# Performance work log

Measured on AMD Instinct MI355X. Metric: run time of the kernel, lower is better.

## Reference

```python
import jax, jax.numpy as jnp
import numpy as np

NEG = jnp.float32(-1e30)  # log-space 'zero' (avoids -inf NaNs)


def _ctc_loss(predictions, targets, pred_lengths, target_lengths, blank=0):
    # predictions: (B, T, C) log-probs; targets: (B, L) int labels (no blanks)
    B, T, C = predictions.shape
    L = targets.shape[1]
    S = 2 * L + 1  # extended label sequence: blank-interleaved

    ext = jnp.full((B, S), blank, dtype=targets.dtype).at[:, 1::2].set(targets)  # (B, S)
    # emission log-prob of each lattice state at each time step: (B, T, S)
    emit = jnp.take_along_axis(
        predictions, jnp.broadcast_to(ext[:, None, :], (B, T, S)), axis=2)

    # skip transition (s-2 -> s) allowed iff ext[s] != blank and ext[s] != ext[s-2]
    ext_m2 = jnp.pad(ext, ((0, 0), (2, 0)), constant_values=-1)[:, :S]
    skip = (ext != blank) & (ext != ext_m2)  # (B, S)

    alpha0 = jnp.full((B, S), NEG, dtype=predictions.dtype)
    alpha0 = alpha0.at[:, 0].set(emit[:, 0, 0]).at[:, 1].set(emit[:, 0, 1])

    emit_t = jnp.swapaxes(emit, 0, 1)  # (T, B, S)
    pad1 = jnp.full((B, 1), NEG, dtype=predictions.dtype)
    pad2 = jnp.full((B, 2), NEG, dtype=predictions.dtype)

    def step(alpha, xs):
        e_t, t = xs
        a1 = alpha
        a2 = jnp.concatenate([pad1, alpha[:, :-1]], axis=1)
        a3 = jnp.where(skip, jnp.concatenate([pad2, alpha[:, :-2]], axis=1), NEG)
        new = jax.nn.logsumexp(jnp.stack([a1, a2, a3], axis=0), axis=0) + e_t
        # freeze lattice beyond each example's input length
        new = jnp.where((t < pred_lengths)[:, None], new, alpha)
        return new, None

    alpha_T, _ = jax.lax.scan(step, alpha0, (emit_t[1:], jnp.arange(1, T)))

    tl = target_lengths.astype(jnp.int32)
    l1 = jnp.take_along_axis(alpha_T, (2 * tl - 1)[:, None], axis=1)[:, 0]
    l2 = jnp.take_along_axis(alpha_T, (2 * tl)[:, None], axis=1)[:, 0]
    per_ex = -jnp.logaddexp(l1, l2)
    # zero_infinity=True
    per_ex = jnp.where(per_ex > jnp.float32(1e29), 0.0, per_ex)
    # reduction='mean': divide by target length, then batch mean
    return jnp.mean(per_ex / jnp.maximum(tl, 1).astype(per_ex.dtype))


def setup_inputs() -> dict:
    key = jax.random.key(0)
    k1, k2, k3 = jax.random.split(key, 3)
    B, T, C, L = 128, 1024, 128, 128
    predictions = jax.random.normal(k1, (B, T, C), dtype=jnp.float32)
    targets = jax.random.randint(k2, (B, L), 1, C, dtype=jnp.int32)  # no blank (=0)
    pred_lengths = jnp.full((B,), T, dtype=jnp.int32)
    target_lengths = jax.random.randint(k3, (B,), L // 2, L + 1, dtype=jnp.int32)
    return {"predictions": predictions, "targets": targets,
            "pred_lengths": pred_lengths, "target_lengths": target_lengths}


def reference(predictions, targets, pred_lengths, target_lengths):
    return _ctc_loss(predictions, targets, pred_lengths, target_lengths, blank=0)
```

## Files before the change

kernel.cpp:

```cpp
#include <hip/hip_runtime.h>


static constexpr float LOG2E_F = 1.4426950408889634f;
static constexpr float LN2_F   = 0.6931471805599453f;
#define NEGF (-1.0e30f)

#if __has_builtin(__builtin_amdgcn_exp2f)
#define FEXP2(x) __builtin_amdgcn_exp2f(x)
#else
#define FEXP2(x) exp2f(x)
#endif
#if __has_builtin(__builtin_amdgcn_logf)
#define FLOG2(x) __builtin_amdgcn_logf(x)
#else
#define FLOG2(x) log2f(x)
#endif

typedef __attribute__((address_space(3))) uint32_t lds_u32_t;
typedef const __attribute__((address_space(1))) uint32_t glb_u32_t;

__device__ __forceinline__ float dpp_shr1(float src, float fill) {
  return __int_as_float(__builtin_amdgcn_update_dpp(
      __float_as_int(fill), __float_as_int(src), 0x138, 0xF, 0xF, false));
}

template <int T, int C, int L>
__global__ __launch_bounds__(64) void ctc_alpha_dpp(
    const float* __restrict__ pred,
    const int*   __restrict__ targets,
    const int*   __restrict__ pred_len,
    const int*   __restrict__ tgt_len,
    float*       __restrict__ per_ex)
{
  constexpr int ROWS    = 64;
  constexpr int CHUNK_F = ROWS * C;
  constexpr int NCH     = T / ROWS;
  constexpr int S       = 2 * L + 1;

  __shared__ float emis[3 * CHUNK_F];
  __shared__ float afin[S];

  const int b = blockIdx.x;
  const int l = threadIdx.x;

  const float* __restrict__ prow = pred + (size_t)b * T * C;
  const int plen = pred_len[b];
  int tl = tgt_len[b]; if (tl < 1) tl = 1; if (tl > L) tl = L;

  const int cc1 = targets[b * L + 2 * l];
  const int cc3 = targets[b * L + 2 * l + 1];
  const bool skip1 = (l == 0) ? false : (cc1 != targets[b * L + 2 * l - 1]);
  const bool skip3 = (cc3 != cc1);

  auto stage = [&](int c) {
    const float* src0 = prow + (size_t)c * CHUNK_F + (l << 2);
    float* dst0 = &emis[(c % 3) * CHUNK_F];
#pragma unroll
    for (int i = 0; i < 32; ++i) {
      __builtin_amdgcn_global_load_lds((glb_u32_t*)(src0 + (i << 8)),
                                       (lds_u32_t*)(dst0 + (i << 8)),
                                       16, 0, 0);
    }
  };

  stage(0); stage(1);
  asm volatile("s_waitcnt vmcnt(32)" ::: "memory");

  float a0 = emis[0] * LOG2E_F;
  float x1 = (l == 0) ? emis[cc1] * LOG2E_F : NEGF;
  float x2 = NEGF, x3 = NEGF, x4 = NEGF;

  const int tmax = plen < T ? plen : T;

  auto step = [&](float rEb, float rE1, float rE3) {
    const float Eb = rEb * LOG2E_F;
    const float E1 = rE1 * LOG2E_F;
    const float E3 = rE3 * LOG2E_F;
    const float P4 = dpp_shr1(x4, a0);
    const float P3 = dpp_shr1(x3, NEGF);
    const float s1 = skip1 ? P3 : NEGF;
    const float m1 = fmaxf(fmaxf(x1, P4), s1);
    const float n1 = m1 + FLOG2(FEXP2(x1 - m1) + FEXP2(P4 - m1) + FEXP2(s1 - m1)) + E1;
    const float m2 = fmaxf(x2, x1);
    const float n2 = m2 + FLOG2(1.0f + FEXP2(-fabsf(x2 - x1))) + Eb;
    const float s3 = skip3 ? x1 : NEGF;
    const float m3 = fmaxf(fmaxf(x3, x2), s3);
    const float n3 = m3 + FLOG2(FEXP2(x3 - m3) + FEXP2(x2 - m3) + FEXP2(s3 - m3)) + E3;
    const float m4 = fmaxf(x4, x3);
    const float n4 = m4 + FLOG2(1.0f + FEXP2(-fabsf(x4 - x3))) + Eb;
    a0 += Eb;
    x1 = n1; x2 = n2; x3 = n3; x4 = n4;
  };

  auto loadg = [&](float (&gb)[8], float (&g1)[8], float (&g3)[8], int r0) {
#pragma unroll
    for (int j = 0; j < 8; ++j) {
      int rr = r0 + j; if (rr > T - 1) rr = T - 1;
      const int rb = ((rr >> 6) % 3) * CHUNK_F + (rr & 63) * C;
      gb[j] = emis[rb];
      g1[j] = emis[rb + cc1];
      g3[j] = emis[rb + cc3];
    }
  };

#pragma unroll
  for (int t = 1; t < 8; ++t) {
    if (t < tmax) {
      const int rb = t * C;
      step(emis[rb], emis[rb + cc1], emis[rb + cc3]);
    }
  }

  float Ab[8], A1[8], A3[8], Bb[8], B1[8], B3[8];
  loadg(Ab, A1, A3, 8);

  for (int t0 = 8; t0 + 16 <= T; t0 += 16) {
    if ((t0 & 63) == 8) {
      const int c = t0 >> 6;
      if (c + 2 < NCH) {
        stage(c + 2);
        asm volatile("s_waitcnt vmcnt(32)" ::: "memory");
      } else {
        asm volatile("s_waitcnt vmcnt(0)" ::: "memory");
      }
    }
    loadg(Bb, B1, B3, t0 + 8);
    if (t0 + 16 <= tmax) {
#pragma unroll
      for (int j = 0; j < 8; ++j) step(Ab[j], A1[j], A3[j]);
      loadg(Ab, A1, A3, t0 + 16);
#pragma unroll
      for (int j = 0; j < 8; ++j) step(Bb[j], B1[j], B3[j]);
    } else {
#pragma unroll
      for (int j = 0; j < 8; ++j)
        if (t0 + j < tmax) step(Ab[j], A1[j], A3[j]);
      loadg(Ab, A1, A3, t0 + 16);
#pragma unroll
      for (int j = 0; j < 8; ++j)
        if (t0 + 8 + j < tmax) step(Bb[j], B1[j], B3[j]);
    }
  }

  afin[4 * l + 1] = x1;
  afin[4 * l + 2] = x2;
  afin[4 * l + 3] = x3;
  afin[4 * l + 4] = x4;
  if (l == 0) afin[0] = a0;
  __syncthreads();
  if (l == 0) {
    const float l1 = afin[2 * tl - 1];
    const float l2 = afin[2 * tl];
    const float mm = fmaxf(l1, l2);
    const float ls = mm + FLOG2(FEXP2(l1 - mm) + FEXP2(l2 - mm));
    float per = -(ls * LN2_F);
    if (!(per < 1e29f)) per = 0.0f;
    per_ex[b] = per / (float)tl;
  }
}

__global__ void ctc_reduce_kernel(const float* __restrict__ per_ex,
                                  float* __restrict__ out, int B)
{
  const int l = threadIdx.x;
  float v = 0.0f;
  for (int i = l; i < B; i += 64) v += per_ex[i];
#pragma unroll
  for (int off = 32; off > 0; off >>= 1) v += __shfl_down(v, off);
  if (l == 0) out[0] = v / (float)B;
}

extern "C" void kernel_launch(void* const* d_in, const int* in_sizes, int n_in,
                              void* d_out, int out_size, void* d_ws, size_t ws_size,
                              hipStream_t stream)
{
  const float* pred    = (const float*)d_in[0];
  const int*   targets = (const int*)d_in[1];
  const int*   plen    = (const int*)d_in[2];
  const int*   tlen    = (const int*)d_in[3];
  float*       out     = (float*)d_out;
  float*       ws      = (float*)d_ws;

  constexpr int B = 128, T = 1024, C = 128, L = 128;

  hipLaunchKernelGGL((ctc_alpha_dpp<T, C, L>), dim3(B), dim3(64), 0, stream,
                     pred, targets, plen, tlen, ws);
  hipLaunchKernelGGL(ctc_reduce_kernel, dim3(1), dim3(64), 0, stream,
                     ws, out, B);
}
```

Before: 218.2 us.

## Run CTC alpha recursion in linear space with per-lane power-of-two exponents

Replaces the log-space logsumexp recursion with linear-probability products and sums. Each lane keeps an integer exponent, and the state is renormalized every 8 steps. Neighbour values arriving over DPP are rescaled by the exponent difference between lanes. This is meant to take the exp2/log2 transcendentals off the serial dependency chain, leaving only the exp of the emissions, which is not on the chain. The cost is extra bookkeeping for the exponents and a risk of underflow or precision loss if scales between lanes differ widely within a renorm window.

```diff
diff --git a/kernel.cpp b/kernel.cpp
--- a/kernel.cpp
+++ b/kernel.cpp
@@ -3,7 +3,6 @@
 
 static constexpr float LOG2E_F = 1.4426950408889634f;
 static constexpr float LN2_F   = 0.6931471805599453f;
-#define NEGF (-1.0e30f)
 
 #if __has_builtin(__builtin_amdgcn_exp2f)
 #define FEXP2(x) __builtin_amdgcn_exp2f(x)
@@ -23,9 +22,12 @@
   return __int_as_float(__builtin_amdgcn_update_dpp(
       __float_as_int(fill), __float_as_int(src), 0x138, 0xF, 0xF, false));
 }
+__device__ __forceinline__ int dpp_shr1_i(int src, int fill) {
+  return __builtin_amdgcn_update_dpp(fill, src, 0x138, 0xF, 0xF, false);
+}
 
 template <int T, int C, int L>
-__global__ __launch_bounds__(64) void ctc_alpha_dpp(
+__global__ __launch_bounds__(64) void ctc_alpha_lin2(
     const float* __restrict__ pred,
     const int*   __restrict__ targets,
     const int*   __restrict__ pred_len,
@@ -49,8 +51,9 @@
 
   const int cc1 = targets[b * L + 2 * l];
   const int cc3 = targets[b * L + 2 * l + 1];
-  const bool skip1 = (l == 0) ? false : (cc1 != targets[b * L + 2 * l - 1]);
-  const bool skip3 = (cc3 != cc1);
+  const float k1 = (l == 0) ? 0.0f
+                  : ((cc1 != targets[b * L + 2 * l - 1]) ? 1.0f : 0.0f);
+  const float k3 = (cc3 != cc1) ? 1.0f : 0.0f;
 
   auto stage = [&](int c) {
     const float* src0 = prow + (size_t)c * CHUNK_F + (l << 2);
@@ -66,30 +69,38 @@
   stage(0); stage(1);
   asm volatile("s_waitcnt vmcnt(32)" ::: "memory");
 
-  float a0 = emis[0] * LOG2E_F;
-  float x1 = (l == 0) ? emis[cc1] * LOG2E_F : NEGF;
-  float x2 = NEGF, x3 = NEGF, x4 = NEGF;
+  float a0 = FEXP2(emis[0] * LOG2E_F);
+  float x1 = (l == 0) ? FEXP2(emis[cc1] * LOG2E_F) : 0.0f;
+  float x2 = 0.0f, x3 = 0.0f, x4 = 0.0f;
+  int   E  = 0;
 
   const int tmax = plen < T ? plen : T;
 
-  auto step = [&](float rEb, float rE1, float rE3) {
-    const float Eb = rEb * LOG2E_F;
-    const float E1 = rE1 * LOG2E_F;
-    const float E3 = rE3 * LOG2E_F;
-    const float P4 = dpp_shr1(x4, a0);
-    const float P3 = dpp_shr1(x3, NEGF);
-    const float s1 = skip1 ? P3 : NEGF;
-    const float m1 = fmaxf(fmaxf(x1, P4), s1);
-    const float n1 = m1 + FLOG2(FEXP2(x1 - m1) + FEXP2(P4 - m1) + FEXP2(s1 - m1)) + E1;
-    const float m2 = fmaxf(x2, x1);
-    const float n2 = m2 + FLOG2(1.0f + FEXP2(-fabsf(x2 - x1))) + Eb;
-    const float s3 = skip3 ? x1 : NEGF;
-    const float m3 = fmaxf(fmaxf(x3, x2), s3);
-    const float n3 = m3 + FLOG2(FEXP2(x3 - m3) + FEXP2(x2 - m3) + FEXP2(s3 - m3)) + E3;
-    const float m4 = fmaxf(x4, x3);
-    const float n4 = m4 + FLOG2(1.0f + FEXP2(-fabsf(x4 - x3))) + Eb;
-    a0 += Eb;
-    x1 = n1; x2 = n2; x3 = n3; x4 = n4;
+  auto step = [&](float Eb, float E1, float E3) {
+    const int Eprev = dpp_shr1_i(E, E);
+    const uint32_t orx = __float_as_uint(x1) | __float_as_uint(x2) |
+                         __float_as_uint(x3) | __float_as_uint(x4);
+    if (orx == 0u) E = Eprev;
+    int dE = Eprev - E;
+    dE = dE < -126 ? -126 : (dE > 126 ? 126 : dE);
+    const float sc = __int_as_float((dE + 127) << 23);
+    const float P4 = dpp_shr1(x4, a0) * sc;
+    const float P3 = dpp_shr1(x3, x3) * sc;
+    const float t1 = fmaf(k1, P3, x1 + P4);
+    const float t2 = x2 + x1;
+    const float t3 = fmaf(k3, x1, x3 + x2);
+    const float t4 = x4 + x3;
+    x1 = t1 * E1; x2 = t2 * Eb; x3 = t3 * E3; x4 = t4 * Eb;
+    a0 *= Eb;
+  };
+
+  auto renorm = [&]() {
+    const float m = fmaxf(fmaxf(fmaxf(x1, x2), fmaxf(x3, x4)), a0);
+    int ebi = (int)((__float_as_uint(m) >> 23) & 0xffu);
+    if (ebi == 0) ebi = 126;
+    const float sc = __uint_as_float((uint32_t)(253 - ebi) << 23);
+    x1 *= sc; x2 *= sc; x3 *= sc; x4 *= sc; a0 *= sc;
+    E += ebi - 126;
   };
 
   auto loadg = [&](float (&gb)[8], float (&g1)[8], float (&g3)[8], int r0) {
@@ -97,25 +108,28 @@
     for (int j = 0; j < 8; ++j) {
       int rr = r0 + j; if (rr > T - 1) rr = T - 1;
       const int rb = ((rr >> 6) % 3) * CHUNK_F + (rr & 63) * C;
-      gb[j] = emis[rb];
-      g1[j] = emis[rb + cc1];
-      g3[j] = emis[rb + cc3];
-    }
-  };
-
-#pragma unroll
-  for (int t = 1; t < 8; ++t) {
+      gb[j] = FEXP2(emis[rb]       * LOG2E_F);
+      g1[j] = FEXP2(emis[rb + cc1] * LOG2E_F);
+      g3[j] = FEXP2(emis[rb + cc3] * LOG2E_F);
+    }
+  };
+
+#pragma unroll
+  for (int t = 1; t < 16; ++t) {
+    if (t == 8) renorm();
     if (t < tmax) {
       const int rb = t * C;
-      step(emis[rb], emis[rb + cc1], emis[rb + cc3]);
+      step(FEXP2(emis[rb]       * LOG2E_F),
+           FEXP2(emis[rb + cc1] * LOG2E_F),
+           FEXP2(emis[rb + cc3] * LOG2E_F));
     }
   }
 
   float Ab[8], A1[8], A3[8], Bb[8], B1[8], B3[8];
-  loadg(Ab, A1, A3, 8);
-
-  for (int t0 = 8; t0 + 16 <= T; t0 += 16) {
-    if ((t0 & 63) == 8) {
+  loadg(Ab, A1, A3, 16);
+
+  for (int t0 = 16; t0 + 16 <= T; t0 += 16) {
+    if ((t0 & 63) == 16) {
       const int c = t0 >> 6;
       if (c + 2 < NCH) {
         stage(c + 2);
@@ -125,10 +139,12 @@
       }
     }
     loadg(Bb, B1, B3, t0 + 8);
+    renorm();
     if (t0 + 16 <= tmax) {
 #pragma unroll
       for (int j = 0; j < 8; ++j) step(Ab[j], A1[j], A3[j]);
       loadg(Ab, A1, A3, t0 + 16);
+      renorm();
 #pragma unroll
       for (int j = 0; j < 8; ++j) step(Bb[j], B1[j], B3[j]);
     } else {
@@ -136,17 +152,19 @@
       for (int j = 0; j < 8; ++j)
         if (t0 + j < tmax) step(Ab[j], A1[j], A3[j]);
       loadg(Ab, A1, A3, t0 + 16);
+      renorm();
 #pragma unroll
       for (int j = 0; j < 8; ++j)
         if (t0 + 8 + j < tmax) step(Bb[j], B1[j], B3[j]);
     }
   }
 
-  afin[4 * l + 1] = x1;
-  afin[4 * l + 2] = x2;
-  afin[4 * l + 3] = x3;
-  afin[4 * l + 4] = x4;
-  if (l == 0) afin[0] = a0;
+  const float fE = (float)E;
+  afin[4 * l + 1] = FLOG2(x1) + fE;
+  afin[4 * l + 2] = FLOG2(x2) + fE;
+  afin[4 * l + 3] = FLOG2(x3) + fE;
+  afin[4 * l + 4] = FLOG2(x4) + fE;
+  if (l == 0) afin[0] = FLOG2(a0) + fE;
   __syncthreads();
   if (l == 0) {
     const float l1 = afin[2 * tl - 1];
@@ -183,7 +201,7 @@
 
   constexpr int B = 128, T = 1024, C = 128, L = 128;
 
-  hipLaunchKernelGGL((ctc_alpha_dpp<T, C, L>), dim3(B), dim3(64), 0, stream,
+  hipLaunchKernelGGL((ctc_alpha_lin2<T, C, L>), dim3(B), dim3(64), 0, stream,
                      pred, targets, plen, tlen, ws);
   hipLaunchKernelGGL(ctc_reduce_kernel, dim3(1), dim3(64), 0, stream,
                      ws, out, B);
```

Result: faster. 193.7 us (-11.2%).
